# Kernel optimization log

Measured on AMD Instinct MI355X. Metric: run time of the kernel, lower is better.

## Reference

```python
import jax, jax.numpy as jnp
import numpy as np

DIM = 192
HEADS = 8
EPS = 1e-12  # torch F.normalize eps


def _l2norm(t):
    # normalize over last axis, matching torch.nn.functional.normalize
    n = jnp.sqrt(jnp.sum(t * t, axis=-1, keepdims=True))
    return t / jnp.maximum(n, EPS)


def setup_inputs() -> dict:
    key = jax.random.key(0)
    k1, k2, k3, k4 = jax.random.split(key, 4)
    B, C, H, W = 16, DIM, 128, 128
    s = 1.0 / np.sqrt(C)
    return {
        "x": jax.random.normal(k1, (B, C, H, W), dtype=jnp.float32),
        "w_qkv": jax.random.normal(k2, (C, 3 * C), dtype=jnp.float32) * s,
        "w_proj": jax.random.normal(k3, (C, C), dtype=jnp.float32) * s,
        "b_proj": jax.random.normal(k4, (C,), dtype=jnp.float32) * 0.01,
        "temperature": jnp.ones((HEADS, 1, 1), dtype=jnp.float32),
    }


def reference(x, w_qkv, w_proj, b_proj, temperature):
    B, C, H, W = x.shape
    N = H * W
    h = HEADS
    d = C // h
    # [B,C,H,W] -> [B,N,C]
    xt = x.reshape(B, C, N).transpose(0, 2, 1)
    qkv = (xt @ w_qkv).reshape(B, N, 3, h, d)
    qkv = qkv.transpose(2, 0, 3, 1, 4)           # [3,B,h,N,d]
    q, k, v = qkv[0], qkv[1], qkv[2]
    # transpose to channel-as-token: [B,h,d,N]
    q = _l2norm(q.transpose(0, 1, 3, 2))
    k = _l2norm(k.transpose(0, 1, 3, 2))
    v = v.transpose(0, 1, 3, 2)
    # small channel attention matrix [B,h,d,d]
    attn = jnp.einsum("bhdn,bhen->bhde", q, k) * temperature
    attn = jax.nn.softmax(attn, axis=-1)
    out = jnp.einsum("bhde,bhen->bhdn", attn, v)  # [B,h,d,N]
    out = out.transpose(0, 3, 1, 2).reshape(B, N, C)
    out = out @ w_proj + b_proj
    return out.transpose(0, 2, 1).reshape(B, C, H, W)
```

## Files before the change

kernel.cpp:

```cpp
#include <hip/hip_runtime.h>
#include <hip/hip_bf16.h>
#include <math.h>

#define C_DIM 192
#define NTOK 16384
#define NB 16
#define NH 8
#define HD 24
#define EPSN 1e-12f

typedef float f32x4 __attribute__((ext_vector_type(4)));
typedef __bf16 bf16x4 __attribute__((ext_vector_type(4)));
typedef __bf16 bf16x8 __attribute__((ext_vector_type(8)));

__device__ __forceinline__ f32x4 mfma16(bf16x8 a, bf16x8 b, f32x4 c) {
  return __builtin_amdgcn_mfma_f32_16x16x32_bf16(a, b, c, 0, 0, 0);
}

__device__ __forceinline__ bf16x8 cvt8(const float* __restrict__ p) {
  f32x4 a = *(const f32x4*)p;
  f32x4 b = *(const f32x4*)(p + 4);
  bf16x8 r;
  r[0] = (__bf16)a[0]; r[1] = (__bf16)a[1]; r[2] = (__bf16)a[2]; r[3] = (__bf16)a[3];
  r[4] = (__bf16)b[0]; r[5] = (__bf16)b[1]; r[6] = (__bf16)b[2]; r[7] = (__bf16)b[3];
  return r;
}

__global__ __launch_bounds__(256, 2) void k1_gram(const float* __restrict__ x,
                                                  __bf16* __restrict__ gpart,
                                                  int kc) {
  const int b = blockIdx.y, chunk = blockIdx.x;
  const float* xb = x + (size_t)b * C_DIM * NTOK + (size_t)chunk * kc;
  __shared__ __bf16 xsh[2][C_DIM * 40];
  const int t = threadIdx.x;
  const int lane = t & 63, wid = t >> 6;
  const int lrow = lane & 15, loct = lane >> 4;
  const int r0 = (wid >> 1) * 96, c0 = (wid & 1) * 96;
  f32x4 acc[6][6] = {};
  f32x4 sA[6], sB[6];
  const int nst = kc >> 5;

#define K1_LOADR(dst, ks)                                                      \
  {                                                                            \
    _Pragma("unroll") for (int it = 0; it < 6; ++it) {                         \
      int idx = it * 256 + t, r = idx >> 3, c8 = idx & 7;                      \
      dst[it] = *(const f32x4*)(xb + (size_t)r * NTOK + (ks) + 4 * c8);        \
    }                                                                          \
  }
#define K1_STORE(buf, src)                                                     \
  {                                                                            \
    _Pragma("unroll") for (int it = 0; it < 6; ++it) {                         \
      int idx = it * 256 + t, r = idx >> 3, c8 = idx & 7;                      \
      bf16x4 w;                                                                \
      w[0] = (__bf16)src[it][0]; w[1] = (__bf16)src[it][1];                    \
      w[2] = (__bf16)src[it][2]; w[3] = (__bf16)src[it][3];                    \
      *(bf16x4*)(&xsh[buf][r * 40 + 4 * c8]) = w;                              \
    }                                                                          \
  }
#define K1_COMP(buf)                                                           \
  {                                                                            \
    bf16x8 fa[6];                                                              \
    _Pragma("unroll") for (int i = 0; i < 6; ++i)                              \
        fa[i] = *(const bf16x8*)(&xsh[buf][(r0 + 16 * i + lrow) * 40 +         \
                                           8 * loct]);                         \
    _Pragma("unroll") for (int j = 0; j < 6; ++j) {                            \
      bf16x8 fb =                                                              \
          *(const bf16x8*)(&xsh[buf][(c0 + 16 * j + lrow) * 40 + 8 * loct]);   \
      _Pragma("unroll") for (int i = 0; i < 6; ++i)                            \
          acc[i][j] = mfma16(fa[i], fb, acc[i][j]);                            \
    }                                                                          \
  }

  K1_LOADR(sA, 0);
  K1_STORE(0, sA);
  K1_LOADR(sB, 32);
  __syncthreads();

  for (int s = 0; s < nst; s += 2) {
    if (s + 2 < nst) K1_LOADR(sA, 32 * (s + 2));
    K1_COMP(0);
    K1_STORE(1, sB);
    __syncthreads();
    if (s + 3 < nst) K1_LOADR(sB, 32 * (s + 3));
    K1_COMP(1);
    if (s + 2 < nst) K1_STORE(0, sA);
    __syncthreads();
  }
#undef K1_LOADR
#undef K1_STORE
#undef K1_COMP

  if (wid != 2) {
    __bf16* gp = gpart + ((size_t)chunk * NB + b) * C_DIM * C_DIM;
#pragma unroll
    for (int i = 0; i < 6; ++i)
#pragma unroll
      for (int j = 0; j < 6; ++j)
#pragma unroll
        for (int e = 0; e < 4; ++e)
          gp[(size_t)(r0 + 16 * i + 4 * loct + e) * C_DIM + (c0 + 16 * j + lrow)] =
              (__bf16)acc[i][j][e];
  }
}

__global__ __launch_bounds__(256) void k2a_reduce(const __bf16* __restrict__ gpart,
                                                  float* __restrict__ G,
                                                  int nchunk) {
  const int qi = blockIdx.y, b = blockIdx.z;
  const int idx = blockIdx.x * 256 + threadIdx.x;
  const int r = idx / 24, c4 = idx % 24;
  const int r_off = (qi == 2) ? 96 : 0;
  const int c_off = (qi == 0) ? 0 : 96;
  const size_t total = (size_t)NB * C_DIM * C_DIM;
  const size_t base = (size_t)b * C_DIM * C_DIM +
                      (size_t)(r_off + r) * C_DIM + c_off + 4 * c4;
  float s0 = 0.f, s1 = 0.f, s2 = 0.f, s3 = 0.f;
  for (int ch = 0; ch < nchunk; ++ch) {
    bf16x4 v = *(const bf16x4*)(gpart + ch * total + base);
    s0 += (float)v[0]; s1 += (float)v[1]; s2 += (float)v[2]; s3 += (float)v[3];
  }
  float* Gb = G + (size_t)b * C_DIM * C_DIM;
  f32x4 sv; sv[0] = s0; sv[1] = s1; sv[2] = s2; sv[3] = s3;
  *(f32x4*)(Gb + (size_t)(r_off + r) * C_DIM + c_off + 4 * c4) = sv;
  if (qi == 1) {
    Gb[(size_t)(96 + 4 * c4 + 0) * C_DIM + r] = s0;
    Gb[(size_t)(96 + 4 * c4 + 1) * C_DIM + r] = s1;
    Gb[(size_t)(96 + 4 * c4 + 2) * C_DIM + r] = s2;
    Gb[(size_t)(96 + 4 * c4 + 3) * C_DIM + r] = s3;
  }
}

__global__ __launch_bounds__(256) void k2b_fused(const float* __restrict__ G,
                                                 const float* __restrict__ wqkv,
                                                 const float* __restrict__ temp,
                                                 float* __restrict__ Yt) {
  const int h = blockIdx.x, b = blockIdx.y;
  __shared__ float Tl[48 * 196];
  __shared__ float SL[32][33];
  __shared__ float qn2L[HD], kn2L[HD];
  const int t = threadIdx.x;
  const int lane = t & 63, wid = t >> 6;
  const int lrow = lane & 15, loct = lane >> 4;
  const float* Gb = G + (size_t)b * C_DIM * C_DIM;

  if (wid < 3) {
    const int p = wid * 16 + lrow;
    const int col = (p < HD) ? (h * HD + p) : (192 + h * HD + p - HD);
    f32x4 acc[12] = {};
    for (int s = 0; s < 6; ++s) {
      bf16x8 fa;
#pragma unroll
      for (int e = 0; e < 8; ++e)
        fa[e] = (__bf16)wqkv[(size_t)(32 * s + 8 * loct + e) * 576 + col];
#pragma unroll
      for (int j = 0; j < 12; ++j) {
        bf16x8 fb = cvt8(Gb + (size_t)(16 * j + lrow) * C_DIM + 32 * s + 8 * loct);
        acc[j] = mfma16(fa, fb, acc[j]);
      }
    }
#pragma unroll
    for (int j = 0; j < 12; ++j)
#pragma unroll
      for (int e = 0; e < 4; ++e)
        Tl[(wid * 16 + 4 * loct + e) * 196 + 16 * j + lrow] = acc[j][e];
  }
  __syncthreads();

  const int r = wid >> 1, j = wid & 1;
  f32x4 acc = {};
  for (int s = 0; s < 6; ++s) {
    bf16x8 fa = cvt8(&Tl[(16 * r + lrow) * 196 + 32 * s + 8 * loct]);
    bf16x8 fb;
#pragma unroll
    for (int e = 0; e < 8; ++e)
      fb[e] = (__bf16)wqkv[(size_t)(32 * s + 8 * loct + e) * 576 + 192 + h * HD +
                           16 * j + lrow];
    acc = mfma16(fa, fb, acc);
  }
#pragma unroll
  for (int e = 0; e < 4; ++e) {
    int d = 16 * r + 4 * loct + e, ee = 16 * j + lrow;
    if (d < HD && ee < HD) SL[d][ee] = acc[e];
  }
  if (t < 48) {
    const int dd = (t < HD) ? t : t - HD;
    const int row = ((t < HD) ? 0 : 192) + h * HD + dd;
    float s = 0.f;
    for (int c = 0; c < C_DIM; ++c)
      s += Tl[t * 196 + c] * wqkv[(size_t)c * 576 + row];
    if (t < HD) qn2L[dd] = s; else kn2L[dd] = s;
  }
  __syncthreads();
  if (t < HD) {
    const float tp = temp[h];
    float nq = fmaxf(sqrtf(fmaxf(qn2L[t], 0.f)), EPSN);
    float lg[HD];
    float m = -1e30f;
#pragma unroll
    for (int e = 0; e < HD; ++e) {
      float nk = fmaxf(sqrtf(fmaxf(kn2L[e], 0.f)), EPSN);
      lg[e] = SL[t][e] / (nq * nk) * tp;
      m = fmaxf(m, lg[e]);
    }
    float sum = 0.f;
#pragma unroll
    for (int e = 0; e < HD; ++e) { lg[e] = __expf(lg[e] - m); sum += lg[e]; }
    float inv = 1.f / sum;
#pragma unroll
    for (int e = 0; e < HD; ++e) SL[t][e] = lg[e] * inv;
  }
  __syncthreads();
  if (t < C_DIM) {
    float wv[HD];
#pragma unroll
    for (int e = 0; e < HD; ++e)
      wv[e] = wqkv[(size_t)t * 576 + 384 + h * HD + e];
    float* Yo = Yt + ((size_t)b * C_DIM + t) * C_DIM + h * HD;
#pragma unroll
    for (int d = 0; d < HD; ++d) {
      float y = 0.f;
#pragma unroll
      for (int e = 0; e < HD; ++e) y += SL[d][e] * wv[e];
      Yo[d] = y;
    }
  }
}

__global__ __launch_bounds__(256) void k2c_m(const float* __restrict__ wproj,
                                             const float* __restrict__ Yt,
                                             __bf16* __restrict__ M) {
  const int b = blockIdx.y, rb = blockIdx.x;
  const int lane = threadIdx.x & 63, wid = threadIdx.x >> 6;
  const int lrow = lane & 15, loct = lane >> 4;
  const float* Yb = Yt + (size_t)b * C_DIM * C_DIM;
  const int coA = rb * 64 + wid * 16 + lrow;
  f32x4 acc[12] = {};
  for (int s = 0; s < 6; ++s) {
    bf16x8 fa;
#pragma unroll
    for (int e = 0; e < 8; ++e)
      fa[e] = (__bf16)wproj[(size_t)(32 * s + 8 * loct + e) * C_DIM + coA];
#pragma unroll
    for (int j = 0; j < 12; ++j) {
      bf16x8 fb = cvt8(Yb + (size_t)(16 * j + lrow) * C_DIM + 32 * s + 8 * loct);
      acc[j] = mfma16(fa, fb, acc[j]);
    }
  }
  __bf16* Mo = M + (size_t)b * C_DIM * C_DIM;
#pragma unroll
  for (int j = 0; j < 12; ++j)
#pragma unroll
    for (int e = 0; e < 4; ++e)
      Mo[(size_t)(rb * 64 + wid * 16 + 4 * loct + e) * C_DIM + 16 * j + lrow] =
          (__bf16)acc[j][e];
}

__global__ __launch_bounds__(256, 3) void k3_out(const float* __restrict__ x,
                                                 const __bf16* __restrict__ M,
                                                 const float* __restrict__ bproj,
                                                 float* __restrict__ out) {
  const int nt = blockIdx.x, half = blockIdx.y, b = blockIdx.z;
  const int rbase = half * 96;
  __shared__ __bf16 Ml[96 * C_DIM];
  __shared__ float biasL[96];
  const int t = threadIdx.x;
  const int lane = t & 63, w = t >> 6;
  const int lrow = lane & 15, loct = lane >> 4;

  const __bf16* Mb = M + (size_t)b * C_DIM * C_DIM + (size_t)rbase * C_DIM;
  for (int i = t; i < 96 * 24; i += 256) {
    int row = i / 24, ch = i % 24;
    bf16x8 v = *(const bf16x8*)(Mb + row * C_DIM + ch * 8);
    *(bf16x8*)(Ml + row * C_DIM + ((ch ^ (row & 7)) * 8)) = v;
  }
  if (t < 96) biasL[t] = bproj[rbase + t];
  __syncthreads();

  const float* xb = x + (size_t)b * C_DIM * NTOK;
  float* ob = out + (size_t)b * C_DIM * NTOK;
  const int n0 = nt * 256 + w * 64;

  f32x4 acc[6][4] = {};
  f32x4 xs4[8];
#pragma unroll
  for (int e = 0; e < 8; ++e)
    xs4[e] = *(const f32x4*)(xb + (size_t)(8 * loct + e) * NTOK + n0 + 4 * lrow);

  for (int s = 0; s < 6; ++s) {
    bf16x8 fb[4];
#pragma unroll
    for (int nf = 0; nf < 4; ++nf)
#pragma unroll
      for (int e = 0; e < 8; ++e)
        fb[nf][e] = (__bf16)xs4[e][nf];
    if (s < 5) {
#pragma unroll
      for (int e = 0; e < 8; ++e)
        xs4[e] = *(const f32x4*)(xb + (size_t)(32 * (s + 1) + 8 * loct + e) * NTOK +
                                 n0 + 4 * lrow);
    }
#pragma unroll
    for (int tt = 0; tt < 6; ++tt) {
      int rowb = 16 * tt + lrow;
      bf16x8 fa = *(const bf16x8*)(Ml + rowb * C_DIM +
                                   (((4 * s + loct) ^ (rowb & 7)) * 8));
#pragma unroll
      for (int nf = 0; nf < 4; ++nf)
        acc[tt][nf] = mfma16(fa, fb[nf], acc[tt][nf]);
    }
  }

  __syncthreads();
  float* epi_w = (float*)Ml + w * 1088;
#pragma unroll
  for (int tt = 0; tt < 6; ++tt) {
    f32x4 bias4 = *(const f32x4*)(biasL + 16 * tt + 4 * loct);
#pragma unroll
    for (int e = 0; e < 4; ++e) {
      f32x4 v;
      v[0] = acc[tt][0][e] + bias4[e];
      v[1] = acc[tt][1][e] + bias4[e];
      v[2] = acc[tt][2][e] + bias4[e];
      v[3] = acc[tt][3][e] + bias4[e];
      *(f32x4*)(epi_w + (4 * loct + e) * 68 + 4 * lrow) = v;
    }
#pragma unroll
    for (int h = 0; h < 4; ++h) {
      int r = 4 * h + loct;
      f32x4 v = *(const f32x4*)(epi_w + r * 68 + 4 * lrow);
      *(f32x4*)(ob + (size_t)(rbase + 16 * tt + r) * NTOK + n0 + 4 * lrow) = v;
    }
  }
}

extern "C" void kernel_launch(void* const* d_in, const int* in_sizes, int n_in,
                              void* d_out, int out_size, void* d_ws, size_t ws_size,
                              hipStream_t stream) {
  const float* x = (const float*)d_in[0];
  const float* wqkv = (const float*)d_in[1];
  const float* wproj = (const float*)d_in[2];
  const float* bproj = (const float*)d_in[3];
  const float* temp = (const float*)d_in[4];
  float* out = (float*)d_out;

  const size_t GSZ = (size_t)NB * C_DIM * C_DIM;
  int nchunk = 32;
  while (nchunk > 1 &&
         (size_t)nchunk * GSZ * 2 + GSZ * 4 + GSZ * 4 + GSZ * 2 > ws_size)
    nchunk >>= 1;
  __bf16* gpart = (__bf16*)d_ws;
  float* G = (float*)(gpart + (size_t)nchunk * GSZ);
  float* Yt = G + GSZ;
  __bf16* M = (__bf16*)(Yt + GSZ);

  k1_gram<<<dim3(nchunk, NB), 256, 0, stream>>>(x, gpart, NTOK / nchunk);
  k2a_reduce<<<dim3(9, 3, NB), 256, 0, stream>>>(gpart, G, nchunk);
  k2b_fused<<<dim3(NH, NB), 256, 0, stream>>>(G, wqkv, temp, Yt);
  k2c_m<<<dim3(3, NB), 256, 0, stream>>>(wproj, Yt, M);
  k3_out<<<dim3(NTOK / 256, 2, NB), 256, 0, stream>>>(x, M, bproj, out);
}
```

Measured before the change: 208.3 us.

## Load Gram-kernel tiles directly to LDS as fp32 with swizzled layout

```diff
diff --git a/kernel.cpp b/kernel.cpp
--- a/kernel.cpp
+++ b/kernel.cpp
@@ -17,13 +17,15 @@
   return __builtin_amdgcn_mfma_f32_16x16x32_bf16(a, b, c, 0, 0, 0);
 }
 
-__device__ __forceinline__ bf16x8 cvt8(const float* __restrict__ p) {
-  f32x4 a = *(const f32x4*)p;
-  f32x4 b = *(const f32x4*)(p + 4);
+__device__ __forceinline__ bf16x8 cvt8_2(f32x4 a, f32x4 b) {
   bf16x8 r;
   r[0] = (__bf16)a[0]; r[1] = (__bf16)a[1]; r[2] = (__bf16)a[2]; r[3] = (__bf16)a[3];
   r[4] = (__bf16)b[0]; r[5] = (__bf16)b[1]; r[6] = (__bf16)b[2]; r[7] = (__bf16)b[3];
   return r;
+}
+
+__device__ __forceinline__ bf16x8 cvt8(const float* __restrict__ p) {
+  return cvt8_2(*(const f32x4*)p, *(const f32x4*)(p + 4));
 }
 
 __global__ __launch_bounds__(256, 2) void k1_gram(const float* __restrict__ x,
@@ -31,63 +33,54 @@
                                                   int kc) {
   const int b = blockIdx.y, chunk = blockIdx.x;
   const float* xb = x + (size_t)b * C_DIM * NTOK + (size_t)chunk * kc;
-  __shared__ __bf16 xsh[2][C_DIM * 40];
+  __shared__ float xsf[2][C_DIM * 32];
   const int t = threadIdx.x;
   const int lane = t & 63, wid = t >> 6;
   const int lrow = lane & 15, loct = lane >> 4;
   const int r0 = (wid >> 1) * 96, c0 = (wid & 1) * 96;
+  const int lx = lrow & 7;
+  const int gl_row = 48 * wid + (lane >> 3);
+  const int gl_sw = 4 * ((lane & 7) ^ (lane >> 3));
   f32x4 acc[6][6] = {};
-  f32x4 sA[6], sB[6];
   const int nst = kc >> 5;
 
-#define K1_LOADR(dst, ks)                                                      \
+#define K1_GLL(buf, ks_)                                                       \
   {                                                                            \
     _Pragma("unroll") for (int it = 0; it < 6; ++it) {                         \
-      int idx = it * 256 + t, r = idx >> 3, c8 = idx & 7;                      \
-      dst[it] = *(const f32x4*)(xb + (size_t)r * NTOK + (ks) + 4 * c8);        \
-    }                                                                          \
-  }
-#define K1_STORE(buf, src)                                                     \
-  {                                                                            \
-    _Pragma("unroll") for (int it = 0; it < 6; ++it) {                         \
-      int idx = it * 256 + t, r = idx >> 3, c8 = idx & 7;                      \
-      bf16x4 w;                                                                \
-      w[0] = (__bf16)src[it][0]; w[1] = (__bf16)src[it][1];                    \
-      w[2] = (__bf16)src[it][2]; w[3] = (__bf16)src[it][3];                    \
-      *(bf16x4*)(&xsh[buf][r * 40 + 4 * c8]) = w;                              \
+      const float* g = xb + (size_t)(gl_row + 8 * it) * NTOK + (ks_) + gl_sw;  \
+      float* l = &xsf[buf][(48 * wid + 8 * it) * 32 + 4 * lane];               \
+      __builtin_amdgcn_global_load_lds(                                        \
+          (const __attribute__((address_space(1))) void*)g,                    \
+          (__attribute__((address_space(3))) void*)l, 16, 0, 0);               \
     }                                                                          \
   }
 #define K1_COMP(buf)                                                           \
   {                                                                            \
+    const int c1 = (2 * loct) ^ lx;                                            \
     bf16x8 fa[6];                                                              \
-    _Pragma("unroll") for (int i = 0; i < 6; ++i)                              \
-        fa[i] = *(const bf16x8*)(&xsh[buf][(r0 + 16 * i + lrow) * 40 +         \
-                                           8 * loct]);                         \
+    _Pragma("unroll") for (int i = 0; i < 6; ++i) {                            \
+      const float* rb_ = &xsf[buf][(r0 + 16 * i + lrow) * 32];                 \
+      fa[i] = cvt8_2(*(const f32x4*)(rb_ + 4 * c1),                            \
+                     *(const f32x4*)(rb_ + 4 * (c1 ^ 1)));                     \
+    }                                                                          \
     _Pragma("unroll") for (int j = 0; j < 6; ++j) {                            \
-      bf16x8 fb =                                                              \
-          *(const bf16x8*)(&xsh[buf][(c0 + 16 * j + lrow) * 40 + 8 * loct]);   \
+      const float* rb_ = &xsf[buf][(c0 + 16 * j + lrow) * 32];                 \
+      bf16x8 fb = cvt8_2(*(const f32x4*)(rb_ + 4 * c1),                        \
+                         *(const f32x4*)(rb_ + 4 * (c1 ^ 1)));                 \
       _Pragma("unroll") for (int i = 0; i < 6; ++i)                            \
           acc[i][j] = mfma16(fa[i], fb, acc[i][j]);                            \
     }                                                                          \
   }
 
-  K1_LOADR(sA, 0);
-  K1_STORE(0, sA);
-  K1_LOADR(sB, 32);
-  __syncthreads();
-
-  for (int s = 0; s < nst; s += 2) {
-    if (s + 2 < nst) K1_LOADR(sA, 32 * (s + 2));
-    K1_COMP(0);
-    K1_STORE(1, sB);
+  K1_GLL(0, 0);
+  __syncthreads();
+  for (int s = 0; s < nst; ++s) {
+    const int cur = s & 1;
+    if (s + 1 < nst) K1_GLL(cur ^ 1, 32 * (s + 1));
+    K1_COMP(cur);
     __syncthreads();
-    if (s + 3 < nst) K1_LOADR(sB, 32 * (s + 3));
-    K1_COMP(1);
-    if (s + 2 < nst) K1_STORE(0, sA);
-    __syncthreads();
-  }
-#undef K1_LOADR
-#undef K1_STORE
+  }
+#undef K1_GLL
 #undef K1_COMP
 
   if (wid != 2) {
@@ -325,10 +318,10 @@
       *(f32x4*)(epi_w + (4 * loct + e) * 68 + 4 * lrow) = v;
     }
 #pragma unroll
-    for (int h = 0; h < 4; ++h) {
-      int r = 4 * h + loct;
-      f32x4 v = *(const f32x4*)(epi_w + r * 68 + 4 * lrow);
-      *(f32x4*)(ob + (size_t)(rbase + 16 * tt + r) * NTOK + n0 + 4 * lrow) = v;
+    for (int hh = 0; hh < 4; ++hh) {
+      int rr = 4 * hh + loct;
+      f32x4 v = *(const f32x4*)(epi_w + rr * 68 + 4 * lrow);
+      *(f32x4*)(ob + (size_t)(rbase + 16 * tt + rr) * NTOK + n0 + 4 * lrow) = v;
     }
   }
 }
```

Result: no change. 206.3 us (-1.0%).
